# Optimization experiments

Hardware: AMD Instinct MI355X
Metric: run time of the kernel (lower is better)

## Reference

```python
import jax, jax.numpy as jnp
import numpy as np
import math

SR = 96000.0
FRAME = 2048
NB = 16
GAIN_RANGE = (-24.0, 24.0)
Q_RANGE = (0.5, 16.0)
BROADBAND = (-60.0, 0.0)
HPF_R = (20.0, 500.0)
LPF_R = (5000.0, 20000.0)
SHELF_R = (50.0, 16000.0)
PEAK_R = (100.0, 15000.0)


def _dfreq(n, rng):
    lo, hi = math.log(rng[0]), math.log(rng[1])
    return jnp.exp(lo + n * (hi - lo))


def _dgain(n, rng=GAIN_RANGE):
    return rng[0] + n * (rng[1] - rng[0])


def _dq(n):
    lo, hi = math.log(Q_RANGE[0]), math.log(Q_RANGE[1])
    return jnp.exp(lo + n * (hi - lo))


def _coeffs(ftype, fc, gain_db, Q):
    # returns stacked [g, k, a1, a2, a3, m0, m1, m2], each same shape as fc
    g = jnp.clip(jnp.tan(math.pi * fc / SR), 1e-6, 100.0)
    Q = jnp.clip(Q, 0.1, 100.0)
    one = jnp.ones_like(g)
    zero = jnp.zeros_like(g)
    if ftype in ('highpass', 'lowpass'):
        k = 1.0 / Q
        a1 = 1.0 / (1.0 + g * (g + k)); a2 = g * a1; a3 = g * a2
        if ftype == 'highpass':
            m0, m1, m2 = one, -k, -one
        else:
            m0, m1, m2 = zero, zero, one
    elif ftype == 'peak':
        A = jnp.power(10.0, gain_db / 40.0)
        k = jnp.where(gain_db >= 0, 1.0 / (Q * A), A / Q)
        a1 = 1.0 / (1.0 + g * (g + k)); a2 = g * a1; a3 = g * a2
        m0, m1, m2 = one, k * (A * A - 1.0), zero
    elif ftype == 'lowshelf':
        A = jnp.power(10.0, gain_db / 40.0); sA = jnp.sqrt(A); k = 1.0 / Q
        gs = jnp.where(gain_db >= 0, g / sA, g * sA)
        a1 = 1.0 / (1.0 + gs * (gs + k)); a2 = gs * a1; a3 = gs * a2
        m0, m1, m2 = one, k * (A - 1.0), A * A - 1.0
    else:  # highshelf
        A = jnp.power(10.0, gain_db / 40.0); sA = jnp.sqrt(A); k = 1.0 / Q
        gs = jnp.where(gain_db >= 0, g * sA, g / sA)
        a1 = 1.0 / (1.0 + gs * (gs + k)); a2 = gs * a1; a3 = gs * a2
        m0, m1, m2 = A * A, k * (1.0 - A) * A, 1.0 - A * A
    return jnp.stack([g, k, a1, a2, a3, m0, m1, m2], 0)


def _all_coeffs(params, n_frames_audio):
    # params: (B, 50, n_frames_params) -> coeffs (nF, NB, 8, B), in/out gains (nF, B)
    B = params.shape[0]
    nFp = params.shape[2]
    pidx = jnp.minimum(jnp.arange(n_frames_audio), nFp - 1)
    fp = jnp.take(params, pidx, axis=2)                 # (B, 50, nF)
    bq = fp[:, :NB * 3, :].reshape(B, NB, 3, n_frames_audio)
    in_g = jnp.power(10.0, _dgain(fp[:, -2, :], BROADBAND) / 20.0)   # (B, nF)
    out_g = jnp.power(10.0, _dgain(fp[:, -1, :], BROADBAND) / 20.0)  # (B, nF)
    cs = []
    for i in range(NB):
        fn, gn, qn = bq[:, i, 0], bq[:, i, 1], bq[:, i, 2]  # (B, nF)
        Q = _dq(qn)
        if i == 0:
            c = _coeffs('highpass', _dfreq(fn, HPF_R), None, Q)
        elif i == 15:
            c = _coeffs('lowpass', _dfreq(fn, LPF_R), None, Q)
        elif i == 1:
            c = _coeffs('lowshelf', _dfreq(fn, SHELF_R), _dgain(gn), Q)
        elif i == 14:
            c = _coeffs('highshelf', _dfreq(fn, SHELF_R), _dgain(gn), Q)
        else:
            c = _coeffs('peak', _dfreq(fn, PEAK_R), _dgain(gn), Q)
        cs.append(c)  # (8, B, nF)
    coeffs = jnp.transpose(jnp.stack(cs, 0), (3, 0, 1, 2))  # (nF, NB, 8, B)
    return coeffs, in_g.T, out_g.T


def _forward(audio, params):
    B, S = audio.shape
    nF = S // FRAME  # S chosen as exact multiple of FRAME
    coeffs, in_g, out_g = _all_coeffs(params, nF)
    frames = jnp.transpose(audio.reshape(B, nF, FRAME), (1, 2, 0))  # (nF, FRAME, B)

    def frame_step(states, xs):
        fr, c, ig, og = xs  # fr (FRAME,B), c (NB,8,B), ig (B,), og (B,)
        x = fr * ig[None, :]
        new_states = []
        for i in range(NB):
            a1, a2, a3 = c[i, 2], c[i, 3], c[i, 4]
            m0, m1, m2 = c[i, 5], c[i, 6], c[i, 7]

            def samp(st, xn, a1=a1, a2=a2, a3=a3, m0=m0, m1=m1, m2=m2):
                ic1, ic2 = st
                v3 = xn - ic2
                v1 = a1 * ic1 + a2 * v3
                v2 = ic2 + a2 * v1 + a3 * v3
                out = m0 * xn + m1 * v1 + m2 * v2
                return (2.0 * v1 - ic1, 2.0 * v2 - ic2), out

            (ic1, ic2), x = jax.lax.scan(samp, (states[i, 0], states[i, 1]), x)
            new_states.append(jnp.stack([ic1, ic2], 0))
        return jnp.stack(new_states, 0), x * og[None, :]

    init = jnp.zeros((NB, 2, B), audio.dtype)
    _, out = jax.lax.scan(frame_step, init, (frames, coeffs, in_g, out_g))
    return jnp.transpose(out, (2, 0, 1)).reshape(B, S)  # (B, S)


_forward_jit = jax.jit(_forward)


def setup_inputs() -> dict:
    key = jax.random.key(0)
    k1, k2 = jax.random.split(key)
    B, S, nFp = 32, 49152, 24  # 24 frames of 2048 samples
    audio = jax.random.normal(k1, (B, S), dtype=jnp.float32) * 0.1
    params = jax.random.uniform(k2, (B, 50, nFp), dtype=jnp.float32)
    return {'audio': audio, 'params': params}


def reference(audio, params):
    return _forward_jit(audio, params)
```

## Files before the change

### kernel.cpp

```cpp
#include <hip/hip_runtime.h>
#include <math.h>

#define NBATCH 32
#define S      49152
#define NF     24
#define NB     16
#define NBLK   4
#define CHUNK  16
#define NCH    768
#define NWAVE  12

__device__ __forceinline__ float clampf(float x, float lo, float hi) {
    return fminf(fmaxf(x, lo), hi);
}

#define FOREACH_S(OP) \
    OP(s00) OP(s01) OP(s02) OP(s03) OP(s04) OP(s05) OP(s06) OP(s07) \
    OP(s08) OP(s09) OP(s10) OP(s11) OP(s12) OP(s13) OP(s14) OP(s15)

#define DECL_S(x) float x;

#define STEPA(x) { \
    const float n1_ = fmaf(t00, ic1, fmaf(t01, ic2, b0 * (x))); \
    const float n2_ = fmaf(t10, ic1, fmaf(t11, ic2, b1 * (x))); \
    ic1 = n1_; ic2 = n2_; }

#define STEPC(x) { \
    const float y_  = fmaf(c0, ic1, fmaf(c1, ic2, c2 * (x))); \
    const float n1_ = fmaf(t00, ic1, fmaf(t01, ic2, b0 * (x))); \
    const float n2_ = fmaf(t10, ic1, fmaf(t11, ic2, b1 * (x))); \
    (x) = y_; ic1 = n1_; ic2 = n2_; }

__global__ __launch_bounds__(NCH, 3)
void biquad_chain_kernel(const float* __restrict__ audio,
                         const float* __restrict__ params,
                         float* __restrict__ out,
                         unsigned int* __restrict__ ws)
{
    __shared__ float sc[NB][NF][16];
    __shared__ float sgain[2][NF];
    __shared__ float4 saggM[NWAVE];
    __shared__ float  saggC[NWAVE][2];
    __shared__ float  sv[NWAVE][2];

    const int t       = threadIdx.x;
    const int xcd     = blockIdx.x & 7;
    const int slot_   = blockIdx.x >> 3;
    const int bt      = xcd * 4 + (slot_ & 3);
    const int quarter = slot_ >> 2;
    const int lane    = t & 63;
    const int wave    = t >> 6;
    const int frame   = quarter * 6 + (wave >> 1);

    if (t < NB * NF) {
        const int f  = t / NF;
        const int fr = t % NF;
        const float* P = params + (size_t)bt * 50 * NF;
        const float fn = P[(3 * f + 0) * NF + fr];
        const float gn = P[(3 * f + 1) * NF + fr];
        const float qn = P[(3 * f + 2) * NF + fr];

        float Q = __expf(-0.69314718f + qn * 3.4657359f);
        Q = clampf(Q, 0.1f, 100.0f);

        float lo, hi;
        int type;
        if      (f == 0)  { lo = 20.0f;   hi = 500.0f;   type = 0; }
        else if (f == 15) { lo = 5000.0f; hi = 20000.0f; type = 1; }
        else if (f == 1)  { lo = 50.0f;   hi = 16000.0f; type = 3; }
        else if (f == 14) { lo = 50.0f;   hi = 16000.0f; type = 4; }
        else              { lo = 100.0f;  hi = 15000.0f; type = 2; }

        const float fc = __expf(__logf(lo) + fn * (__logf(hi) - __logf(lo)));
        float g_ = __tanf((float)M_PI * fc / 96000.0f);
        g_ = clampf(g_, 1e-6f, 100.0f);
        const float gdb = -24.0f + 48.0f * gn;

        float a1, a2, a3, m0, m1, m2;
        if (type == 0 || type == 1) {
            const float k = 1.0f / Q;
            a1 = 1.0f / (1.0f + g_ * (g_ + k)); a2 = g_ * a1; a3 = g_ * a2;
            if (type == 0) { m0 = 1.0f; m1 = -k;   m2 = -1.0f; }
            else           { m0 = 0.0f; m1 = 0.0f; m2 = 1.0f;  }
        } else if (type == 2) {
            const float A = __expf(gdb * (2.30258509f / 40.0f));
            const float k = (gdb >= 0.0f) ? 1.0f / (Q * A) : A / Q;
            a1 = 1.0f / (1.0f + g_ * (g_ + k)); a2 = g_ * a1; a3 = g_ * a2;
            m0 = 1.0f; m1 = k * (A * A - 1.0f); m2 = 0.0f;
        } else {
            const float A  = __expf(gdb * (2.30258509f / 40.0f));
            const float sA = sqrtf(A);
            const float k  = 1.0f / Q;
            float gs;
            if (type == 3) gs = (gdb >= 0.0f) ? g_ / sA : g_ * sA;
            else           gs = (gdb >= 0.0f) ? g_ * sA : g_ / sA;
            a1 = 1.0f / (1.0f + gs * (gs + k)); a2 = gs * a1; a3 = gs * a2;
            if (type == 3) { m0 = 1.0f;  m1 = k * (A - 1.0f);      m2 = A * A - 1.0f; }
            else           { m0 = A * A; m1 = k * (1.0f - A) * A;  m2 = 1.0f - A * A; }
        }

        const float q2  = a2 * a2 + a3;
        const float t00 = 2.0f * a1 - 1.0f;
        const float t01 = -2.0f * a2;
        const float t10 = 2.0f * a1 * a2;
        const float t11 = 1.0f - 2.0f * q2;
        const float b0  = 2.0f * a2;
        const float b1  = 2.0f * q2;
        const float c0  = a1 * (m1 + m2 * a2);
        const float c1  = m2 * (1.0f - q2) - m1 * a2;
        const float c2  = m0 + m1 * a2 + m2 * q2;

        float u00 = t00, u01 = t01, u10 = t10, u11 = t11;
        #pragma unroll
        for (int i = 0; i < 4; i++) {
            const float n00 = u00 * u00 + u01 * u10;
            const float n01 = u00 * u01 + u01 * u11;
            const float n10 = u10 * u00 + u11 * u10;
            const float n11 = u10 * u01 + u11 * u11;
            u00 = n00; u01 = n01; u10 = n10; u11 = n11;
        }

        sc[f][fr][0] = t00; sc[f][fr][1] = t01; sc[f][fr][2] = t10; sc[f][fr][3] = t11;
        sc[f][fr][4] = b0;  sc[f][fr][5] = b1;  sc[f][fr][6] = c0;  sc[f][fr][7] = c1;
        sc[f][fr][8] = c2;  sc[f][fr][9] = u00; sc[f][fr][10] = u01; sc[f][fr][11] = u10;
        sc[f][fr][12] = u11;
    }
    if (t >= 384 && t < 384 + 2 * NF) {
        const int idx = t - 384;
        const int which = idx / NF;
        const int fr    = idx % NF;
        const float* P = params + (size_t)bt * 50 * NF;
        const float p  = P[(48 + which) * NF + fr];
        const float db = -60.0f + 60.0f * p;
        sgain[which][fr] = __expf(db * (2.30258509f / 20.0f));
    }
    __syncthreads();

    FOREACH_S(DECL_S)
    {
        const float ing = sgain[0][frame];
        const float* base = audio + (size_t)bt * S
                          + (size_t)(quarter * NCH + t) * CHUNK;
        float4 q;
        q = *(const float4*)(base +  0); s00 = q.x*ing; s01 = q.y*ing; s02 = q.z*ing; s03 = q.w*ing;
        q = *(const float4*)(base +  4); s04 = q.x*ing; s05 = q.y*ing; s06 = q.z*ing; s07 = q.w*ing;
        q = *(const float4*)(base +  8); s08 = q.x*ing; s09 = q.y*ing; s10 = q.z*ing; s11 = q.w*ing;
        q = *(const float4*)(base + 12); s12 = q.x*ing; s13 = q.y*ing; s14 = q.z*ing; s15 = q.w*ing;
    }

    #pragma unroll 1
    for (int f = 0; f < NB; f++) {
        const float4 q0 = *(const float4*)&sc[f][frame][0];
        const float4 q1 = *(const float4*)&sc[f][frame][4];
        const float4 q2 = *(const float4*)&sc[f][frame][8];
        const float  M11v = sc[f][frame][12];
        const float t00 = q0.x, t01 = q0.y, t10 = q0.z, t11 = q0.w;
        const float b0  = q1.x, b1  = q1.y, c0  = q1.z, c1  = q1.w;
        const float c2  = q2.x;

        float ic1 = 0.0f, ic2 = 0.0f;
        FOREACH_S(STEPA)

        float Md00 = q2.y, Md01 = q2.z, Md10 = q2.w, Md11 = M11v;
        float Ac0 = ic1, Ac1 = ic2;
        #pragma unroll
        for (int d = 1; d < 64; d <<= 1) {
            const float lc0 = __shfl_up(Ac0, d);
            const float lc1 = __shfl_up(Ac1, d);
            if (lane >= d) {
                Ac0 = fmaf(Md00, lc0, fmaf(Md01, lc1, Ac0));
                Ac1 = fmaf(Md10, lc0, fmaf(Md11, lc1, Ac1));
            }
            const float n00 = Md00 * Md00 + Md01 * Md10;
            const float n01 = Md00 * Md01 + Md01 * Md11;
            const float n10 = Md10 * Md00 + Md11 * Md10;
            const float n11 = Md10 * Md01 + Md11 * Md11;
            Md00 = n00; Md01 = n01; Md10 = n10; Md11 = n11;
        }

        if (lane == 63) {
            saggM[wave] = make_float4(Md00, Md01, Md10, Md11);
            saggC[wave][0] = Ac0; saggC[wave][1] = Ac1;
        }
        __syncthreads();

        const unsigned int tag = (unsigned int)(f + 1);
        unsigned int* stagebase = ws + ((bt * NB + f) * NBLK) * 8;

        if (wave == 0) {
            float G00 = 1.0f, G01 = 0.0f, G10 = 0.0f, G11 = 1.0f, Gc0 = 0.0f, Gc1 = 0.0f;
            if (lane < NWAVE) {
                const float4 m = saggM[lane];
                G00 = m.x; G01 = m.y; G10 = m.z; G11 = m.w;
                Gc0 = saggC[lane][0]; Gc1 = saggC[lane][1];
            }
            #pragma unroll
            for (int d = 1; d < 16; d <<= 1) {
                const float l00 = __shfl_up(G00, d);
                const float l01 = __shfl_up(G01, d);
                const float l10 = __shfl_up(G10, d);
                const float l11 = __shfl_up(G11, d);
                const float lc0 = __shfl_up(Gc0, d);
                const float lc1 = __shfl_up(Gc1, d);
                if (lane >= d && lane < NWAVE) {
                    const float n00 = G00 * l00 + G01 * l10;
                    const float n01 = G00 * l01 + G01 * l11;
                    const float n10 = G10 * l00 + G11 * l10;
                    const float n11 = G10 * l01 + G11 * l11;
                    const float nc0 = G00 * lc0 + G01 * lc1 + Gc0;
                    const float nc1 = G10 * lc0 + G11 * lc1 + Gc1;
                    G00 = n00; G01 = n01; G10 = n10; G11 = n11;
                    Gc0 = nc0; Gc1 = nc1;
                }
            }

            if (quarter < NBLK - 1 && lane == NWAVE - 1) {
                unsigned int* slot = stagebase + quarter * 8;
                float* dp = (float*)(slot + 1);
                __hip_atomic_store(&dp[0], G00, __ATOMIC_RELAXED, __HIP_MEMORY_SCOPE_AGENT);
                __hip_atomic_store(&dp[1], G01, __ATOMIC_RELAXED, __HIP_MEMORY_SCOPE_AGENT);
                __hip_atomic_store(&dp[2], G10, __ATOMIC_RELAXED, __HIP_MEMORY_SCOPE_AGENT);
                __hip_atomic_store(&dp[3], G11, __ATOMIC_RELAXED, __HIP_MEMORY_SCOPE_AGENT);
                __hip_atomic_store(&dp[4], Gc0, __ATOMIC_RELAXED, __HIP_MEMORY_SCOPE_AGENT);
                __hip_atomic_store(&dp[5], Gc1, __ATOMIC_RELAXED, __HIP_MEMORY_SCOPE_AGENT);
                __hip_atomic_store(slot, tag, __ATOMIC_RELEASE, __HIP_MEMORY_SCOPE_AGENT);
            }

            float P00 = __shfl_up(G00, 1);
            float P01 = __shfl_up(G01, 1);
            float P10 = __shfl_up(G10, 1);
            float P11 = __shfl_up(G11, 1);
            float Pc0 = __shfl_up(Gc0, 1);
            float Pc1 = __shfl_up(Gc1, 1);
            if (lane == 0) { P00 = 1.0f; P01 = 0.0f; P10 = 0.0f; P11 = 1.0f; Pc0 = 0.0f; Pc1 = 0.0f; }

            float S0x = 0.0f, S0y = 0.0f;
            if (lane == 0 && quarter > 0) {
                float sx = 0.0f, sy = 0.0f;
                for (int k2 = 0; k2 < quarter; k2++) {
                    unsigned int* slot = stagebase + k2 * 8;
                    while (__hip_atomic_load(slot, __ATOMIC_ACQUIRE, __HIP_MEMORY_SCOPE_AGENT) != tag) {
                        __builtin_amdgcn_s_sleep(1);
                    }
                    float* dp = (float*)(slot + 1);
                    const float m00 = __hip_atomic_load(&dp[0], __ATOMIC_RELAXED, __HIP_MEMORY_SCOPE_AGENT);
                    const float m01 = __hip_atomic_load(&dp[1], __ATOMIC_RELAXED, __HIP_MEMORY_SCOPE_AGENT);
                    const float m10 = __hip_atomic_load(&dp[2], __ATOMIC_RELAXED, __HIP_MEMORY_SCOPE_AGENT);
                    const float m11 = __hip_atomic_load(&dp[3], __ATOMIC_RELAXED, __HIP_MEMORY_SCOPE_AGENT);
                    const float cc0 = __hip_atomic_load(&dp[4], __ATOMIC_RELAXED, __HIP_MEMORY_SCOPE_AGENT);
                    const float cc1 = __hip_atomic_load(&dp[5], __ATOMIC_RELAXED, __HIP_MEMORY_SCOPE_AGENT);
                    const float nx = m00 * sx + m01 * sy + cc0;
                    const float ny = m10 * sx + m11 * sy + cc1;
                    sx = nx; sy = ny;
                }
                S0x = sx; S0y = sy;
            }
            S0x = __shfl(S0x, 0);
            S0y = __shfl(S0y, 0);

            if (lane < NWAVE) {
                sv[lane][0] = fmaf(P00, S0x, fmaf(P01, S0y, Pc0));
                sv[lane][1] = fmaf(P10, S0x, fmaf(P11, S0y, Pc1));
            }
        }
        __syncthreads();

        const float vx = sv[wave][0];
        const float vy = sv[wave][1];

        float ce0 = __shfl_up(Ac0, 1);
        float ce1 = __shfl_up(Ac1, 1);
        if (lane == 0) { ce0 = 0.0f; ce1 = 0.0f; }

        float w0 = vx, w1 = vy;
        float p00 = q2.y, p01 = q2.z, p10 = q2.w, p11 = M11v;
        #pragma unroll
        for (int b = 0; b < 6; b++) {
            if (lane & (1 << b)) {
                const float nw0 = fmaf(p00, w0, p01 * w1);
                const float nw1 = fmaf(p10, w0, p11 * w1);
                w0 = nw0; w1 = nw1;
            }
            if (b < 5) {
                const float n00 = p00 * p00 + p01 * p10;
                const float n01 = p00 * p01 + p01 * p11;
                const float n10 = p10 * p00 + p11 * p10;
                const float n11 = p10 * p01 + p11 * p11;
                p00 = n00; p01 = n01; p10 = n10; p11 = n11;
            }
        }
        ic1 = w0 + ce0;
        ic2 = w1 + ce1;

        FOREACH_S(STEPC)
    }

    {
        const float og = sgain[1][frame];
        float* base = out + (size_t)bt * S + (size_t)(quarter * NCH + t) * CHUNK;
        float4 q;
        q.x = s00*og; q.y = s01*og; q.z = s02*og; q.w = s03*og; *(float4*)(base +  0) = q;
        q.x = s04*og; q.y = s05*og; q.z = s06*og; q.w = s07*og; *(float4*)(base +  4) = q;
        q.x = s08*og; q.y = s09*og; q.z = s10*og; q.w = s11*og; *(float4*)(base +  8) = q;
        q.x = s12*og; q.y = s13*og; q.z = s14*og; q.w = s15*og; *(float4*)(base + 12) = q;
    }
}

extern "C" void kernel_launch(void* const* d_in, const int* in_sizes, int n_in,
                              void* d_out, int out_size, void* d_ws, size_t ws_size,
                              hipStream_t stream)
{
    const float* audio  = (const float*)d_in[0];
    const float* params = (const float*)d_in[1];
    float* out = (float*)d_out;
    unsigned int* ws = (unsigned int*)d_ws;
    biquad_chain_kernel<<<NBLK * NBATCH, NCH, 0, stream>>>(audio, params, out, ws);
}
```

Before: 124.8 us.

## Replicate cross-wave scan in every wave to drop a block barrier per filter stage

Every wave now redundantly runs the 12-element wave-aggregate scan and the cross-block spin-wait itself, instead of wave 0 doing it and broadcasting through shared memory with a second __syncthreads. The aggregate buffers are double-buffered by stage parity so the next stage's writes cannot race with reads. This removes one block-wide barrier per stage and its serialization, at the cost of redundant shuffle math and all 12 waves polling the global flag slots.

Result: slower. 349.6 us (+180.1%).

```diff
diff --git a/kernel.cpp b/kernel.cpp
--- a/kernel.cpp
+++ b/kernel.cpp
@@ -39,9 +39,8 @@
 {
     __shared__ float sc[NB][NF][16];
     __shared__ float sgain[2][NF];
-    __shared__ float4 saggM[NWAVE];
-    __shared__ float  saggC[NWAVE][2];
-    __shared__ float  sv[NWAVE][2];
+    __shared__ float4 saggM[2][NWAVE];
+    __shared__ float  saggC[2][NWAVE][2];
 
     const int t       = threadIdx.x;
     const int xcd     = blockIdx.x & 7;
@@ -150,6 +149,7 @@
 
     #pragma unroll 1
     for (int f = 0; f < NB; f++) {
+        const int buf = f & 1;
         const float4 q0 = *(const float4*)&sc[f][frame][0];
         const float4 q1 = *(const float4*)&sc[f][frame][4];
         const float4 q2 = *(const float4*)&sc[f][frame][8];
@@ -179,94 +179,85 @@
         }
 
         if (lane == 63) {
-            saggM[wave] = make_float4(Md00, Md01, Md10, Md11);
-            saggC[wave][0] = Ac0; saggC[wave][1] = Ac1;
+            saggM[buf][wave] = make_float4(Md00, Md01, Md10, Md11);
+            saggC[buf][wave][0] = Ac0; saggC[buf][wave][1] = Ac1;
         }
         __syncthreads();
+
+        float G00 = 1.0f, G01 = 0.0f, G10 = 0.0f, G11 = 1.0f, Gc0 = 0.0f, Gc1 = 0.0f;
+        if (lane < NWAVE) {
+            const float4 m = saggM[buf][lane];
+            G00 = m.x; G01 = m.y; G10 = m.z; G11 = m.w;
+            Gc0 = saggC[buf][lane][0]; Gc1 = saggC[buf][lane][1];
+        }
+        #pragma unroll
+        for (int d = 1; d < 16; d <<= 1) {
+            const float l00 = __shfl_up(G00, d);
+            const float l01 = __shfl_up(G01, d);
+            const float l10 = __shfl_up(G10, d);
+            const float l11 = __shfl_up(G11, d);
+            const float lc0 = __shfl_up(Gc0, d);
+            const float lc1 = __shfl_up(Gc1, d);
+            if (lane >= d && lane < NWAVE) {
+                const float n00 = G00 * l00 + G01 * l10;
+                const float n01 = G00 * l01 + G01 * l11;
+                const float n10 = G10 * l00 + G11 * l10;
+                const float n11 = G10 * l01 + G11 * l11;
+                const float nc0 = G00 * lc0 + G01 * lc1 + Gc0;
+                const float nc1 = G10 * lc0 + G11 * lc1 + Gc1;
+                G00 = n00; G01 = n01; G10 = n10; G11 = n11;
+                Gc0 = nc0; Gc1 = nc1;
+            }
+        }
 
         const unsigned int tag = (unsigned int)(f + 1);
         unsigned int* stagebase = ws + ((bt * NB + f) * NBLK) * 8;
 
-        if (wave == 0) {
-            float G00 = 1.0f, G01 = 0.0f, G10 = 0.0f, G11 = 1.0f, Gc0 = 0.0f, Gc1 = 0.0f;
-            if (lane < NWAVE) {
-                const float4 m = saggM[lane];
-                G00 = m.x; G01 = m.y; G10 = m.z; G11 = m.w;
-                Gc0 = saggC[lane][0]; Gc1 = saggC[lane][1];
-            }
-            #pragma unroll
-            for (int d = 1; d < 16; d <<= 1) {
-                const float l00 = __shfl_up(G00, d);
-                const float l01 = __shfl_up(G01, d);
-                const float l10 = __shfl_up(G10, d);
-                const float l11 = __shfl_up(G11, d);
-                const float lc0 = __shfl_up(Gc0, d);
-                const float lc1 = __shfl_up(Gc1, d);
-                if (lane >= d && lane < NWAVE) {
-                    const float n00 = G00 * l00 + G01 * l10;
-                    const float n01 = G00 * l01 + G01 * l11;
-                    const float n10 = G10 * l00 + G11 * l10;
-                    const float n11 = G10 * l01 + G11 * l11;
-                    const float nc0 = G00 * lc0 + G01 * lc1 + Gc0;
-                    const float nc1 = G10 * lc0 + G11 * lc1 + Gc1;
-                    G00 = n00; G01 = n01; G10 = n10; G11 = n11;
-                    Gc0 = nc0; Gc1 = nc1;
-                }
-            }
-
-            if (quarter < NBLK - 1 && lane == NWAVE - 1) {
-                unsigned int* slot = stagebase + quarter * 8;
-                float* dp = (float*)(slot + 1);
-                __hip_atomic_store(&dp[0], G00, __ATOMIC_RELAXED, __HIP_MEMORY_SCOPE_AGENT);
-                __hip_atomic_store(&dp[1], G01, __ATOMIC_RELAXED, __HIP_MEMORY_SCOPE_AGENT);
-                __hip_atomic_store(&dp[2], G10, __ATOMIC_RELAXED, __HIP_MEMORY_SCOPE_AGENT);
-                __hip_atomic_store(&dp[3], G11, __ATOMIC_RELAXED, __HIP_MEMORY_SCOPE_AGENT);
-                __hip_atomic_store(&dp[4], Gc0, __ATOMIC_RELAXED, __HIP_MEMORY_SCOPE_AGENT);
-                __hip_atomic_store(&dp[5], Gc1, __ATOMIC_RELAXED, __HIP_MEMORY_SCOPE_AGENT);
-                __hip_atomic_store(slot, tag, __ATOMIC_RELEASE, __HIP_MEMORY_SCOPE_AGENT);
-            }
-
-            float P00 = __shfl_up(G00, 1);
-            float P01 = __shfl_up(G01, 1);
-            float P10 = __shfl_up(G10, 1);
-            float P11 = __shfl_up(G11, 1);
-            float Pc0 = __shfl_up(Gc0, 1);
-            float Pc1 = __shfl_up(Gc1, 1);
-            if (lane == 0) { P00 = 1.0f; P01 = 0.0f; P10 = 0.0f; P11 = 1.0f; Pc0 = 0.0f; Pc1 = 0.0f; }
-
-            float S0x = 0.0f, S0y = 0.0f;
-            if (lane == 0 && quarter > 0) {
-                float sx = 0.0f, sy = 0.0f;
-                for (int k2 = 0; k2 < quarter; k2++) {
-                    unsigned int* slot = stagebase + k2 * 8;
-                    while (__hip_atomic_load(slot, __ATOMIC_ACQUIRE, __HIP_MEMORY_SCOPE_AGENT) != tag) {
-                        __builtin_amdgcn_s_sleep(1);
-                    }
-                    float* dp = (float*)(slot + 1);
-                    const float m00 = __hip_atomic_load(&dp[0], __ATOMIC_RELAXED, __HIP_MEMORY_SCOPE_AGENT);
-                    const float m01 = __hip_atomic_load(&dp[1], __ATOMIC_RELAXED, __HIP_MEMORY_SCOPE_AGENT);
-                    const float m10 = __hip_atomic_load(&dp[2], __ATOMIC_RELAXED, __HIP_MEMORY_SCOPE_AGENT);
-                    const float m11 = __hip_atomic_load(&dp[3], __ATOMIC_RELAXED, __HIP_MEMORY_SCOPE_AGENT);
-                    const float cc0 = __hip_atomic_load(&dp[4], __ATOMIC_RELAXED, __HIP_MEMORY_SCOPE_AGENT);
-                    const float cc1 = __hip_atomic_load(&dp[5], __ATOMIC_RELAXED, __HIP_MEMORY_SCOPE_AGENT);
-                    const float nx = m00 * sx + m01 * sy + cc0;
-                    const float ny = m10 * sx + m11 * sy + cc1;
-                    sx = nx; sy = ny;
-                }
-                S0x = sx; S0y = sy;
-            }
-            S0x = __shfl(S0x, 0);
-            S0y = __shfl(S0y, 0);
-
-            if (lane < NWAVE) {
-                sv[lane][0] = fmaf(P00, S0x, fmaf(P01, S0y, Pc0));
-                sv[lane][1] = fmaf(P10, S0x, fmaf(P11, S0y, Pc1));
-            }
-        }
-        __syncthreads();
-
-        const float vx = sv[wave][0];
-        const float vy = sv[wave][1];
+        if (wave == 0 && quarter < NBLK - 1 && lane == NWAVE - 1) {
+            unsigned int* slot = stagebase + quarter * 8;
+            float* dp = (float*)(slot + 1);
+            __hip_atomic_store(&dp[0], G00, __ATOMIC_RELAXED, __HIP_MEMORY_SCOPE_AGENT);
+            __hip_atomic_store(&dp[1], G01, __ATOMIC_RELAXED, __HIP_MEMORY_SCOPE_AGENT);
+            __hip_atomic_store(&dp[2], G10, __ATOMIC_RELAXED, __HIP_MEMORY_SCOPE_AGENT);
+            __hip_atomic_store(&dp[3], G11, __ATOMIC_RELAXED, __HIP_MEMORY_SCOPE_AGENT);
+            __hip_atomic_store(&dp[4], Gc0, __ATOMIC_RELAXED, __HIP_MEMORY_SCOPE_AGENT);
+            __hip_atomic_store(&dp[5], Gc1, __ATOMIC_RELAXED, __HIP_MEMORY_SCOPE_AGENT);
+            __hip_atomic_store(slot, tag, __ATOMIC_RELEASE, __HIP_MEMORY_SCOPE_AGENT);
+        }
+
+        float S0x = 0.0f, S0y = 0.0f;
+        for (int k2 = 0; k2 < quarter; k2++) {
+            unsigned int* slot = stagebase + k2 * 8;
+            while (__hip_atomic_load(slot, __ATOMIC_ACQUIRE, __HIP_MEMORY_SCOPE_AGENT) != tag) {
+                __builtin_amdgcn_s_sleep(1);
+            }
+            float* dp = (float*)(slot + 1);
+            const float m00 = __hip_atomic_load(&dp[0], __ATOMIC_RELAXED, __HIP_MEMORY_SCOPE_AGENT);
+            const float m01 = __hip_atomic_load(&dp[1], __ATOMIC_RELAXED, __HIP_MEMORY_SCOPE_AGENT);
+            const float m10 = __hip_atomic_load(&dp[2], __ATOMIC_RELAXED, __HIP_MEMORY_SCOPE_AGENT);
+            const float m11 = __hip_atomic_load(&dp[3], __ATOMIC_RELAXED, __HIP_MEMORY_SCOPE_AGENT);
+            const float cc0 = __hip_atomic_load(&dp[4], __ATOMIC_RELAXED, __HIP_MEMORY_SCOPE_AGENT);
+            const float cc1 = __hip_atomic_load(&dp[5], __ATOMIC_RELAXED, __HIP_MEMORY_SCOPE_AGENT);
+            const float nx = m00 * S0x + m01 * S0y + cc0;
+            const float ny = m10 * S0x + m11 * S0y + cc1;
+            S0x = nx; S0y = ny;
+        }
+
+        float Pm00 = 1.0f, Pm01 = 0.0f, Pm10 = 0.0f, Pm11 = 1.0f;
+        float Pc0 = 0.0f, Pc1 = 0.0f;
+        {
+            const int wsrc = (wave > 0) ? (wave - 1) : 0;
+            const float a = __shfl(G00, wsrc);
+            const float b = __shfl(G01, wsrc);
+            const float c = __shfl(G10, wsrc);
+            const float dd = __shfl(G11, wsrc);
+            const float e = __shfl(Gc0, wsrc);
+            const float g2 = __shfl(Gc1, wsrc);
+            if (wave > 0) { Pm00 = a; Pm01 = b; Pm10 = c; Pm11 = dd; Pc0 = e; Pc1 = g2; }
+        }
+
+        const float vx = Pm00 * S0x + Pm01 * S0y + Pc0;
+        const float vy = Pm10 * S0x + Pm11 * S0y + Pc1;
 
         float ce0 = __shfl_up(Ac0, 1);
         float ce1 = __shfl_up(Ac1, 1);
```

## Split biquad chain into per-frame pass, state relay, and replay pass

Applied to the files above, without the earlier changes.

Replaces the single kernel, whose blocks pass filter state through cross-block atomic spin-waits, with three launches. A first per-frame pass (768 blocks of 256 threads) computes each frame's zero-state end states and a 32x32 state-transition matrix built by repeated block-triangular squaring. A small relay kernel then chains those across frames per batch, and a second per-frame pass replays each frame from its correct initial state. This removes the serial inter-block dependency and raises parallelism, at the cost of running the filter cascade twice, extra workspace traffic, and the matrix build. The old kernel is kept as a fallback when the workspace is too small.

After: 140.8 us. 12.8% more time.

```diff
diff --git a/kernel.cpp b/kernel.cpp
--- a/kernel.cpp
+++ b/kernel.cpp
@@ -4,44 +4,354 @@
 #define NBATCH 32
 #define S      49152
 #define NF     24
+#define FRAME  2048
 #define NB     16
-#define NBLK   4
-#define CHUNK  16
-#define NCH    768
-#define NWAVE  12
+#define TPB    256
+#define FCHUNK 8
+
+#define WS_A_ELEMS (NBATCH * NF * 1024)
+#define WS_B_ELEMS (NBATCH * NF * 32)
+#define WS_S_ELEMS (NBATCH * NF * 32)
 
 __device__ __forceinline__ float clampf(float x, float lo, float hi) {
     return fminf(fmaxf(x, lo), hi);
 }
 
-#define FOREACH_S(OP) \
-    OP(s00) OP(s01) OP(s02) OP(s03) OP(s04) OP(s05) OP(s06) OP(s07) \
-    OP(s08) OP(s09) OP(s10) OP(s11) OP(s12) OP(s13) OP(s14) OP(s15)
-
+__device__ __forceinline__ void filter_coeffs(int f, float fn, float gn, float qn,
+                                              float* dst )
+{
+    float Q = __expf(-0.69314718f + qn * 3.4657359f);
+    Q = clampf(Q, 0.1f, 100.0f);
+
+    float lo, hi; int type;
+    if      (f == 0)  { lo = 20.0f;   hi = 500.0f;   type = 0; }
+    else if (f == 15) { lo = 5000.0f; hi = 20000.0f; type = 1; }
+    else if (f == 1)  { lo = 50.0f;   hi = 16000.0f; type = 3; }
+    else if (f == 14) { lo = 50.0f;   hi = 16000.0f; type = 4; }
+    else              { lo = 100.0f;  hi = 15000.0f; type = 2; }
+
+    const float fc = __expf(__logf(lo) + fn * (__logf(hi) - __logf(lo)));
+    float g_ = __tanf((float)M_PI * fc / 96000.0f);
+    g_ = clampf(g_, 1e-6f, 100.0f);
+    const float gdb = -24.0f + 48.0f * gn;
+
+    float a1, a2, a3, m0, m1, m2;
+    if (type == 0 || type == 1) {
+        const float k = 1.0f / Q;
+        a1 = 1.0f / (1.0f + g_ * (g_ + k)); a2 = g_ * a1; a3 = g_ * a2;
+        if (type == 0) { m0 = 1.0f; m1 = -k;   m2 = -1.0f; }
+        else           { m0 = 0.0f; m1 = 0.0f; m2 = 1.0f;  }
+    } else if (type == 2) {
+        const float A = __expf(gdb * (2.30258509f / 40.0f));
+        const float k = (gdb >= 0.0f) ? 1.0f / (Q * A) : A / Q;
+        a1 = 1.0f / (1.0f + g_ * (g_ + k)); a2 = g_ * a1; a3 = g_ * a2;
+        m0 = 1.0f; m1 = k * (A * A - 1.0f); m2 = 0.0f;
+    } else {
+        const float A  = __expf(gdb * (2.30258509f / 40.0f));
+        const float sA = sqrtf(A);
+        const float k  = 1.0f / Q;
+        float gs;
+        if (type == 3) gs = (gdb >= 0.0f) ? g_ / sA : g_ * sA;
+        else           gs = (gdb >= 0.0f) ? g_ * sA : g_ / sA;
+        a1 = 1.0f / (1.0f + gs * (gs + k)); a2 = gs * a1; a3 = gs * a2;
+        if (type == 3) { m0 = 1.0f;  m1 = k * (A - 1.0f);      m2 = A * A - 1.0f; }
+        else           { m0 = A * A; m1 = k * (1.0f - A) * A;  m2 = 1.0f - A * A; }
+    }
+
+    const float q2 = a2 * a2 + a3;
+    dst[0] = 2.0f * a1 - 1.0f;
+    dst[1] = -2.0f * a2;
+    dst[2] = 2.0f * a1 * a2;
+    dst[3] = 1.0f - 2.0f * q2;
+    dst[4] = 2.0f * a2;
+    dst[5] = 2.0f * q2;
+    dst[6] = a1 * (m1 + m2 * a2);
+    dst[7] = m2 * (1.0f - q2) - m1 * a2;
+    dst[8] = m0 + m1 * a2 + m2 * q2;
+    float u00 = dst[0], u01 = dst[1], u10 = dst[2], u11 = dst[3];
+    #pragma unroll
+    for (int i = 0; i < 3; i++) {
+        const float n00 = u00*u00 + u01*u10;
+        const float n01 = u00*u01 + u01*u11;
+        const float n10 = u10*u00 + u11*u10;
+        const float n11 = u10*u01 + u11*u11;
+        u00=n00; u01=n01; u10=n10; u11=n11;
+    }
+    dst[9] = u00; dst[10] = u01; dst[11] = u10; dst[12] = u11;
+}
+
+#define FOREACH_S8(OP) \
+    OP(s00) OP(s01) OP(s02) OP(s03) OP(s04) OP(s05) OP(s06) OP(s07)
 #define DECL_S(x) float x;
-
 #define STEPA(x) { \
     const float n1_ = fmaf(t00, ic1, fmaf(t01, ic2, b0 * (x))); \
     const float n2_ = fmaf(t10, ic1, fmaf(t11, ic2, b1 * (x))); \
     ic1 = n1_; ic2 = n2_; }
-
 #define STEPC(x) { \
     const float y_  = fmaf(c0, ic1, fmaf(c1, ic2, c2 * (x))); \
     const float n1_ = fmaf(t00, ic1, fmaf(t01, ic2, b0 * (x))); \
     const float n2_ = fmaf(t10, ic1, fmaf(t11, ic2, b1 * (x))); \
     (x) = y_; ic1 = n1_; ic2 = n2_; }
 
-__global__ __launch_bounds__(NCH, 3)
-void biquad_chain_kernel(const float* __restrict__ audio,
-                         const float* __restrict__ params,
-                         float* __restrict__ out,
-                         unsigned int* __restrict__ ws)
+__global__ __launch_bounds__(TPB)
+void frame_pass(const float* __restrict__ audio,
+                const float* __restrict__ params,
+                float* __restrict__ out,
+                float* __restrict__ wsA,
+                float* __restrict__ wsB,
+                const float* __restrict__ wsS,
+                int mode)
+{
+    __shared__ float  sf[NB][16];
+    __shared__ float  sg[2];
+    __shared__ float  cAgg[2][4][2];
+    __shared__ float  bfl[NB][2];
+    __shared__ float  sinl[32];
+    __shared__ float4 Mtx[2][16][16];
+
+    const int t    = threadIdx.x;
+    const int blk  = blockIdx.x;
+    const int bt   = blk / NF;
+    const int fr   = blk % NF;
+    const int lane = t & 63;
+    const int wave = t >> 6;
+
+    if (t < NB) {
+        const float* P = params + (size_t)bt * 50 * NF;
+        const float fn = P[(3 * t + 0) * NF + fr];
+        const float gn = P[(3 * t + 1) * NF + fr];
+        const float qn = P[(3 * t + 2) * NF + fr];
+        filter_coeffs(t, fn, gn, qn, sf[t]);
+    }
+    if (t == 16 || t == 17) {
+        const int which = t - 16;
+        const float* P = params + (size_t)bt * 50 * NF;
+        const float p  = P[(48 + which) * NF + fr];
+        sg[which] = __expf((-60.0f + 60.0f * p) * (2.30258509f / 20.0f));
+    }
+    if (mode == 1 && t >= 32 && t < 64) {
+        sinl[t - 32] = wsS[(size_t)(bt * NF + fr) * 32 + (t - 32)];
+    }
+    __syncthreads();
+
+    FOREACH_S8(DECL_S)
+    {
+        const float ing = sg[0];
+        const float* base = audio + (size_t)bt * S + (size_t)fr * FRAME
+                          + (size_t)t * FCHUNK;
+        float4 q;
+        q = *(const float4*)(base + 0); s00 = q.x*ing; s01 = q.y*ing; s02 = q.z*ing; s03 = q.w*ing;
+        q = *(const float4*)(base + 4); s04 = q.x*ing; s05 = q.y*ing; s06 = q.z*ing; s07 = q.w*ing;
+    }
+
+    #pragma unroll 1
+    for (int f = 0; f < NB; f++) {
+        const int buf = f & 1;
+        const float4 q0 = *(const float4*)&sf[f][0];
+        const float4 q1 = *(const float4*)&sf[f][4];
+        const float4 q2 = *(const float4*)&sf[f][8];
+        const float  m811 = sf[f][12];
+        const float t00 = q0.x, t01 = q0.y, t10 = q0.z, t11 = q0.w;
+        const float b0  = q1.x, b1  = q1.y, c0  = q1.z, c1  = q1.w;
+        const float c2  = q2.x;
+
+        float ic1 = 0.0f, ic2 = 0.0f;
+        FOREACH_S8(STEPA)
+
+        float Md00 = q2.y, Md01 = q2.z, Md10 = q2.w, Md11 = m811;
+        float Ac0 = ic1, Ac1 = ic2;
+        #pragma unroll
+        for (int d = 1; d < 64; d <<= 1) {
+            const float lc0 = __shfl_up(Ac0, d);
+            const float lc1 = __shfl_up(Ac1, d);
+            if (lane >= d) {
+                Ac0 = fmaf(Md00, lc0, fmaf(Md01, lc1, Ac0));
+                Ac1 = fmaf(Md10, lc0, fmaf(Md11, lc1, Ac1));
+            }
+            const float n00 = Md00*Md00 + Md01*Md10;
+            const float n01 = Md00*Md01 + Md01*Md11;
+            const float n10 = Md10*Md00 + Md11*Md10;
+            const float n11 = Md10*Md01 + Md11*Md11;
+            Md00=n00; Md01=n01; Md10=n10; Md11=n11;
+        }
+
+        if (lane == 63) { cAgg[buf][wave][0] = Ac0; cAgg[buf][wave][1] = Ac1; }
+        __syncthreads();
+
+        float u0, u1;
+        if (mode == 1) { u0 = sinl[2*f]; u1 = sinl[2*f+1]; }
+        else           { u0 = 0.0f;      u1 = 0.0f;        }
+        for (int j = 0; j < wave; j++) {
+            const float cj0 = cAgg[buf][j][0];
+            const float cj1 = cAgg[buf][j][1];
+            const float n0 = fmaf(Md00, u0, fmaf(Md01, u1, cj0));
+            const float n1 = fmaf(Md10, u0, fmaf(Md11, u1, cj1));
+            u0 = n0; u1 = n1;
+        }
+
+        if (mode == 0 && t == 0) {
+            float z0 = 0.0f, z1 = 0.0f;
+            #pragma unroll
+            for (int j = 0; j < 4; j++) {
+                const float n0 = fmaf(Md00, z0, fmaf(Md01, z1, cAgg[buf][j][0]));
+                const float n1 = fmaf(Md10, z0, fmaf(Md11, z1, cAgg[buf][j][1]));
+                z0 = n0; z1 = n1;
+            }
+            bfl[f][0] = z0; bfl[f][1] = z1;
+        }
+
+        float ce0 = __shfl_up(Ac0, 1);
+        float ce1 = __shfl_up(Ac1, 1);
+        if (lane == 0) { ce0 = 0.0f; ce1 = 0.0f; }
+
+        float w0 = u0, w1 = u1;
+        float p00 = q2.y, p01 = q2.z, p10 = q2.w, p11 = m811;
+        #pragma unroll
+        for (int b = 0; b < 6; b++) {
+            if (lane & (1 << b)) {
+                const float n0 = fmaf(p00, w0, p01 * w1);
+                const float n1 = fmaf(p10, w0, p11 * w1);
+                w0 = n0; w1 = n1;
+            }
+            if (b < 5) {
+                const float n00 = p00*p00 + p01*p10;
+                const float n01 = p00*p01 + p01*p11;
+                const float n10 = p10*p00 + p11*p10;
+                const float n11 = p10*p01 + p11*p11;
+                p00=n00; p01=n01; p10=n10; p11=n11;
+            }
+        }
+        ic1 = w0 + ce0;
+        ic2 = w1 + ce1;
+
+        FOREACH_S8(STEPC)
+    }
+    __syncthreads();
+
+    if (mode == 1) {
+        const float og = sg[1];
+        float* base = out + (size_t)bt * S + (size_t)fr * FRAME + (size_t)t * FCHUNK;
+        float4 q;
+        q.x = s00*og; q.y = s01*og; q.z = s02*og; q.w = s03*og; *(float4*)(base + 0) = q;
+        q.x = s04*og; q.y = s05*og; q.z = s06*og; q.w = s07*og; *(float4*)(base + 4) = q;
+        return;
+    }
+
+    if (t < 32) wsB[(size_t)(bt * NF + fr) * 32 + t] = bfl[t >> 1][t & 1];
+
+    if (fr < NF - 1) {
+        int ii = -1, jj = 0;
+        if (t < 136) {
+            int rem = t;
+            for (int r = 0; r < 16; r++) {
+                if (rem < r + 1) { ii = r; jj = rem; break; }
+                rem -= r + 1;
+            }
+        }
+        if (ii >= 0) {
+            float4 blkv;
+            if (ii == jj) {
+                blkv = make_float4(sf[ii][0], sf[ii][1], sf[ii][2], sf[ii][3]);
+            } else {
+                float pc2 = 1.0f;
+                for (int k = jj + 1; k < ii; k++) pc2 *= sf[k][8];
+                const float w0 = pc2 * sf[jj][6];
+                const float w1 = pc2 * sf[jj][7];
+                blkv = make_float4(sf[ii][4]*w0, sf[ii][4]*w1, sf[ii][5]*w0, sf[ii][5]*w1);
+            }
+            Mtx[0][ii][jj] = blkv;
+        }
+        __syncthreads();
+
+        #pragma unroll 1
+        for (int it = 0; it < 11; it++) {
+            const int rb = it & 1;
+            if (ii >= 0) {
+                float a00 = 0.0f, a01 = 0.0f, a10 = 0.0f, a11 = 0.0f;
+                for (int k = jj; k <= ii; k++) {
+                    const float4 L = Mtx[rb][ii][k];
+                    const float4 R = Mtx[rb][k][jj];
+                    a00 += L.x*R.x + L.y*R.z;
+                    a01 += L.x*R.y + L.y*R.w;
+                    a10 += L.z*R.x + L.w*R.z;
+                    a11 += L.z*R.y + L.w*R.w;
+                }
+                Mtx[rb ^ 1][ii][jj] = make_float4(a00, a01, a10, a11);
+            }
+            __syncthreads();
+        }
+
+        float* Aout = wsA + (size_t)(bt * NF + fr) * 1024;
+        #pragma unroll
+        for (int e = 0; e < 4; e++) {
+            const int idx = t * 4 + e;
+            const int r = idx >> 5, c = idx & 31;
+            float v = 0.0f;
+            if ((r >> 1) >= (c >> 1)) {
+                const float4 bb = Mtx[1][r >> 1][c >> 1];
+                v = (r & 1) ? ((c & 1) ? bb.w : bb.z) : ((c & 1) ? bb.y : bb.x);
+            }
+            Aout[idx] = v;
+        }
+    }
+}
+
+__global__ __launch_bounds__(64)
+void relay_kernel(const float* __restrict__ wsA,
+                  const float* __restrict__ wsB,
+                  float* __restrict__ wsS)
+{
+    const int bt = blockIdx.x;
+    const int l  = threadIdx.x;
+    const int lr = l & 31;
+
+    float s = 0.0f;
+    #pragma unroll 1
+    for (int k = 0; k < NF; k++) {
+        if (l < 32) wsS[(size_t)(bt * NF + k) * 32 + l] = s;
+        if (k == NF - 1) break;
+        const float* Ar = wsA + (size_t)(bt * NF + k) * 1024 + lr * 32;
+        const float4 r0 = *(const float4*)(Ar +  0);
+        const float4 r1 = *(const float4*)(Ar +  4);
+        const float4 r2 = *(const float4*)(Ar +  8);
+        const float4 r3 = *(const float4*)(Ar + 12);
+        const float4 r4 = *(const float4*)(Ar + 16);
+        const float4 r5 = *(const float4*)(Ar + 20);
+        const float4 r6 = *(const float4*)(Ar + 24);
+        const float4 r7 = *(const float4*)(Ar + 28);
+        float acc = wsB[(size_t)(bt * NF + k) * 32 + lr];
+        acc += r0.x*__shfl(s, 0) + r0.y*__shfl(s, 1) + r0.z*__shfl(s, 2) + r0.w*__shfl(s, 3);
+        acc += r1.x*__shfl(s, 4) + r1.y*__shfl(s, 5) + r1.z*__shfl(s, 6) + r1.w*__shfl(s, 7);
+        acc += r2.x*__shfl(s, 8) + r2.y*__shfl(s, 9) + r2.z*__shfl(s,10) + r2.w*__shfl(s,11);
+        acc += r3.x*__shfl(s,12) + r3.y*__shfl(s,13) + r3.z*__shfl(s,14) + r3.w*__shfl(s,15);
+        acc += r4.x*__shfl(s,16) + r4.y*__shfl(s,17) + r4.z*__shfl(s,18) + r4.w*__shfl(s,19);
+        acc += r5.x*__shfl(s,20) + r5.y*__shfl(s,21) + r5.z*__shfl(s,22) + r5.w*__shfl(s,23);
+        acc += r6.x*__shfl(s,24) + r6.y*__shfl(s,25) + r6.z*__shfl(s,26) + r6.w*__shfl(s,27);
+        acc += r7.x*__shfl(s,28) + r7.y*__shfl(s,29) + r7.z*__shfl(s,30) + r7.w*__shfl(s,31);
+        s = acc;
+    }
+}
+
+#define FB_NBLK  4
+#define FB_CHUNK 16
+#define FB_NCH   768
+#define FB_NWAVE 12
+
+#define FOREACH_S16(OP) \
+    OP(s00) OP(s01) OP(s02) OP(s03) OP(s04) OP(s05) OP(s06) OP(s07) \
+    OP(s08) OP(s09) OP(s10) OP(s11) OP(s12) OP(s13) OP(s14) OP(s15)
+
+__global__ __launch_bounds__(FB_NCH, 3)
+void biquad_fallback(const float* __restrict__ audio,
+                     const float* __restrict__ params,
+                     float* __restrict__ out,
+                     unsigned int* __restrict__ ws)
 {
     __shared__ float sc[NB][NF][16];
     __shared__ float sgain[2][NF];
-    __shared__ float4 saggM[NWAVE];
-    __shared__ float  saggC[NWAVE][2];
-    __shared__ float  sv[NWAVE][2];
+    __shared__ float4 saggM[FB_NWAVE];
+    __shared__ float  saggC[FB_NWAVE][2];
+    __shared__ float  sv[FB_NWAVE][2];
 
     const int t       = threadIdx.x;
     const int xcd     = blockIdx.x & 7;
@@ -56,74 +366,17 @@
         const int f  = t / NF;
         const int fr = t % NF;
         const float* P = params + (size_t)bt * 50 * NF;
-        const float fn = P[(3 * f + 0) * NF + fr];
-        const float gn = P[(3 * f + 1) * NF + fr];
-        const float qn = P[(3 * f + 2) * NF + fr];
-
-        float Q = __expf(-0.69314718f + qn * 3.4657359f);
-        Q = clampf(Q, 0.1f, 100.0f);
-
-        float lo, hi;
-        int type;
-        if      (f == 0)  { lo = 20.0f;   hi = 500.0f;   type = 0; }
-        else if (f == 15) { lo = 5000.0f; hi = 20000.0f; type = 1; }
-        else if (f == 1)  { lo = 50.0f;   hi = 16000.0f; type = 3; }
-        else if (f == 14) { lo = 50.0f;   hi = 16000.0f; type = 4; }
-        else              { lo = 100.0f;  hi = 15000.0f; type = 2; }
-
-        const float fc = __expf(__logf(lo) + fn * (__logf(hi) - __logf(lo)));
-        float g_ = __tanf((float)M_PI * fc / 96000.0f);
-        g_ = clampf(g_, 1e-6f, 100.0f);
-        const float gdb = -24.0f + 48.0f * gn;
-
-        float a1, a2, a3, m0, m1, m2;
-        if (type == 0 || type == 1) {
-            const float k = 1.0f / Q;
-            a1 = 1.0f / (1.0f + g_ * (g_ + k)); a2 = g_ * a1; a3 = g_ * a2;
-            if (type == 0) { m0 = 1.0f; m1 = -k;   m2 = -1.0f; }
-            else           { m0 = 0.0f; m1 = 0.0f; m2 = 1.0f;  }
-        } else if (type == 2) {
-            const float A = __expf(gdb * (2.30258509f / 40.0f));
-            const float k = (gdb >= 0.0f) ? 1.0f / (Q * A) : A / Q;
-            a1 = 1.0f / (1.0f + g_ * (g_ + k)); a2 = g_ * a1; a3 = g_ * a2;
-            m0 = 1.0f; m1 = k * (A * A - 1.0f); m2 = 0.0f;
-        } else {
-            const float A  = __expf(gdb * (2.30258509f / 40.0f));
-            const float sA = sqrtf(A);
-            const float k  = 1.0f / Q;
-            float gs;
-            if (type == 3) gs = (gdb >= 0.0f) ? g_ / sA : g_ * sA;
-            else           gs = (gdb >= 0.0f) ? g_ * sA : g_ / sA;
-            a1 = 1.0f / (1.0f + gs * (gs + k)); a2 = gs * a1; a3 = gs * a2;
-            if (type == 3) { m0 = 1.0f;  m1 = k * (A - 1.0f);      m2 = A * A - 1.0f; }
-            else           { m0 = A * A; m1 = k * (1.0f - A) * A;  m2 = 1.0f - A * A; }
-        }
-
-        const float q2  = a2 * a2 + a3;
-        const float t00 = 2.0f * a1 - 1.0f;
-        const float t01 = -2.0f * a2;
-        const float t10 = 2.0f * a1 * a2;
-        const float t11 = 1.0f - 2.0f * q2;
-        const float b0  = 2.0f * a2;
-        const float b1  = 2.0f * q2;
-        const float c0  = a1 * (m1 + m2 * a2);
-        const float c1  = m2 * (1.0f - q2) - m1 * a2;
-        const float c2  = m0 + m1 * a2 + m2 * q2;
-
-        float u00 = t00, u01 = t01, u10 = t10, u11 = t11;
-        #pragma unroll
-        for (int i = 0; i < 4; i++) {
-            const float n00 = u00 * u00 + u01 * u10;
-            const float n01 = u00 * u01 + u01 * u11;
-            const float n10 = u10 * u00 + u11 * u10;
-            const float n11 = u10 * u01 + u11 * u11;
-            u00 = n00; u01 = n01; u10 = n10; u11 = n11;
-        }
-
-        sc[f][fr][0] = t00; sc[f][fr][1] = t01; sc[f][fr][2] = t10; sc[f][fr][3] = t11;
-        sc[f][fr][4] = b0;  sc[f][fr][5] = b1;  sc[f][fr][6] = c0;  sc[f][fr][7] = c1;
-        sc[f][fr][8] = c2;  sc[f][fr][9] = u00; sc[f][fr][10] = u01; sc[f][fr][11] = u10;
-        sc[f][fr][12] = u11;
+        float tmp[13];
+        filter_coeffs(f, P[(3*f+0)*NF+fr], P[(3*f+1)*NF+fr], P[(3*f+2)*NF+fr], tmp);
+        float u00 = tmp[9], u01 = tmp[10], u10 = tmp[11], u11 = tmp[12];
+        const float n00 = u00*u00 + u01*u10;
+        const float n01 = u00*u01 + u01*u11;
+        const float n10 = u10*u00 + u11*u10;
+        const float n11 = u10*u01 + u11*u11;
+        sc[f][fr][0]=tmp[0]; sc[f][fr][1]=tmp[1]; sc[f][fr][2]=tmp[2]; sc[f][fr][3]=tmp[3];
+        sc[f][fr][4]=tmp[4]; sc[f][fr][5]=tmp[5]; sc[f][fr][6]=tmp[6]; sc[f][fr][7]=tmp[7];
+        sc[f][fr][8]=tmp[8]; sc[f][fr][9]=n00; sc[f][fr][10]=n01; sc[f][fr][11]=n10;
+        sc[f][fr][12]=n11;
     }
     if (t >= 384 && t < 384 + 2 * NF) {
         const int idx = t - 384;
@@ -131,16 +384,14 @@
         const int fr    = idx % NF;
         const float* P = params + (size_t)bt * 50 * NF;
         const float p  = P[(48 + which) * NF + fr];
-        const float db = -60.0f + 60.0f * p;
-        sgain[which][fr] = __expf(db * (2.30258509f / 20.0f));
+        sgain[which][fr] = __expf((-60.0f + 60.0f * p) * (2.30258509f / 20.0f));
     }
     __syncthreads();
 
-    FOREACH_S(DECL_S)
+    FOREACH_S16(DECL_S)
     {
         const float ing = sgain[0][frame];
-        const float* base = audio + (size_t)bt * S
-                          + (size_t)(quarter * NCH + t) * CHUNK;
+        const float* base = audio + (size_t)bt * S + (size_t)(quarter * FB_NCH + t) * FB_CHUNK;
         float4 q;
         q = *(const float4*)(base +  0); s00 = q.x*ing; s01 = q.y*ing; s02 = q.z*ing; s03 = q.w*ing;
         q = *(const float4*)(base +  4); s04 = q.x*ing; s05 = q.y*ing; s06 = q.z*ing; s07 = q.w*ing;
@@ -159,7 +410,7 @@
         const float c2  = q2.x;
 
         float ic1 = 0.0f, ic2 = 0.0f;
-        FOREACH_S(STEPA)
+        FOREACH_S16(STEPA)
 
         float Md00 = q2.y, Md01 = q2.z, Md10 = q2.w, Md11 = M11v;
         float Ac0 = ic1, Ac1 = ic2;
@@ -171,11 +422,11 @@
                 Ac0 = fmaf(Md00, lc0, fmaf(Md01, lc1, Ac0));
                 Ac1 = fmaf(Md10, lc0, fmaf(Md11, lc1, Ac1));
             }
-            const float n00 = Md00 * Md00 + Md01 * Md10;
-            const float n01 = Md00 * Md01 + Md01 * Md11;
-            const float n10 = Md10 * Md00 + Md11 * Md10;
-            const float n11 = Md10 * Md01 + Md11 * Md11;
-            Md00 = n00; Md01 = n01; Md10 = n10; Md11 = n11;
+            const float n00 = Md00*Md00 + Md01*Md10;
+            const float n01 = Md00*Md01 + Md01*Md11;
+            const float n10 = Md10*Md00 + Md11*Md10;
+            const float n11 = Md10*Md01 + Md11*Md11;
+            Md00=n00; Md01=n01; Md10=n10; Md11=n11;
         }
 
         if (lane == 63) {
@@ -185,11 +436,11 @@
         __syncthreads();
 
         const unsigned int tag = (unsigned int)(f + 1);
-        unsigned int* stagebase = ws + ((bt * NB + f) * NBLK) * 8;
+        unsigned int* stagebase = ws + ((bt * NB + f) * FB_NBLK) * 8;
 
         if (wave == 0) {
             float G00 = 1.0f, G01 = 0.0f, G10 = 0.0f, G11 = 1.0f, Gc0 = 0.0f, Gc1 = 0.0f;
-            if (lane < NWAVE) {
+            if (lane < FB_NWAVE) {
                 const float4 m = saggM[lane];
                 G00 = m.x; G01 = m.y; G10 = m.z; G11 = m.w;
                 Gc0 = saggC[lane][0]; Gc1 = saggC[lane][1];
@@ -202,19 +453,18 @@
                 const float l11 = __shfl_up(G11, d);
                 const float lc0 = __shfl_up(Gc0, d);
                 const float lc1 = __shfl_up(Gc1, d);
-                if (lane >= d && lane < NWAVE) {
-                    const float n00 = G00 * l00 + G01 * l10;
-                    const float n01 = G00 * l01 + G01 * l11;
-                    const float n10 = G10 * l00 + G11 * l10;
-                    const float n11 = G10 * l01 + G11 * l11;
-                    const float nc0 = G00 * lc0 + G01 * lc1 + Gc0;
-                    const float nc1 = G10 * lc0 + G11 * lc1 + Gc1;
-                    G00 = n00; G01 = n01; G10 = n10; G11 = n11;
-                    Gc0 = nc0; Gc1 = nc1;
+                if (lane >= d && lane < FB_NWAVE) {
+                    const float n00 = G00*l00 + G01*l10;
+                    const float n01 = G00*l01 + G01*l11;
+                    const float n10 = G10*l00 + G11*l10;
+                    const float n11 = G10*l01 + G11*l11;
+                    const float nc0 = G00*lc0 + G01*lc1 + Gc0;
+                    const float nc1 = G10*lc0 + G11*lc1 + Gc1;
+                    G00=n00; G01=n01; G10=n10; G11=n11; Gc0=nc0; Gc1=nc1;
                 }
             }
 
-            if (quarter < NBLK - 1 && lane == NWAVE - 1) {
+            if (quarter < FB_NBLK - 1 && lane == FB_NWAVE - 1) {
                 unsigned int* slot = stagebase + quarter * 8;
                 float* dp = (float*)(slot + 1);
                 __hip_atomic_store(&dp[0], G00, __ATOMIC_RELAXED, __HIP_MEMORY_SCOPE_AGENT);
@@ -258,7 +508,7 @@
             S0x = __shfl(S0x, 0);
             S0y = __shfl(S0y, 0);
 
-            if (lane < NWAVE) {
+            if (lane < FB_NWAVE) {
                 sv[lane][0] = fmaf(P00, S0x, fmaf(P01, S0y, Pc0));
                 sv[lane][1] = fmaf(P10, S0x, fmaf(P11, S0y, Pc1));
             }
@@ -282,22 +532,22 @@
                 w0 = nw0; w1 = nw1;
             }
             if (b < 5) {
-                const float n00 = p00 * p00 + p01 * p10;
-                const float n01 = p00 * p01 + p01 * p11;
-                const float n10 = p10 * p00 + p11 * p10;
-                const float n11 = p10 * p01 + p11 * p11;
-                p00 = n00; p01 = n01; p10 = n10; p11 = n11;
+                const float n00 = p00*p00 + p01*p10;
+                const float n01 = p00*p01 + p01*p11;
+                const float n10 = p10*p00 + p11*p10;
+                const float n11 = p10*p01 + p11*p11;
+                p00=n00; p01=n01; p10=n10; p11=n11;
             }
         }
         ic1 = w0 + ce0;
         ic2 = w1 + ce1;
 
-        FOREACH_S(STEPC)
+        FOREACH_S16(STEPC)
     }
 
     {
         const float og = sgain[1][frame];
-        float* base = out + (size_t)bt * S + (size_t)(quarter * NCH + t) * CHUNK;
+        float* base = out + (size_t)bt * S + (size_t)(quarter * FB_NCH + t) * FB_CHUNK;
         float4 q;
         q.x = s00*og; q.y = s01*og; q.z = s02*og; q.w = s03*og; *(float4*)(base +  0) = q;
         q.x = s04*og; q.y = s05*og; q.z = s06*og; q.w = s07*og; *(float4*)(base +  4) = q;
@@ -313,6 +563,17 @@
     const float* audio  = (const float*)d_in[0];
     const float* params = (const float*)d_in[1];
     float* out = (float*)d_out;
-    unsigned int* ws = (unsigned int*)d_ws;
-    biquad_chain_kernel<<<NBLK * NBATCH, NCH, 0, stream>>>(audio, params, out, ws);
+
+    const size_t needed = ((size_t)WS_A_ELEMS + WS_B_ELEMS + WS_S_ELEMS) * sizeof(float);
+    if (ws_size >= needed) {
+        float* wsA = (float*)d_ws;
+        float* wsB = wsA + WS_A_ELEMS;
+        float* wsS = wsB + WS_B_ELEMS;
+        frame_pass<<<NBATCH * NF, TPB, 0, stream>>>(audio, params, out, wsA, wsB, wsS, 0);
+        relay_kernel<<<NBATCH, 64, 0, stream>>>(wsA, wsB, wsS);
+        frame_pass<<<NBATCH * NF, TPB, 0, stream>>>(audio, params, out, wsA, wsB, wsS, 1);
+    } else {
+        biquad_fallback<<<FB_NBLK * NBATCH, FB_NCH, 0, stream>>>(
+            audio, params, out, (unsigned int*)d_ws);
+    }
 }
```
